# Performance work log

Measured on AMD Instinct MI355X. Metric: run time of the kernel, lower is better.

Reference implementation:

```python
import jax, jax.numpy as jnp
import numpy as np

H, W = 512, 512
G = 8192
ALPHA_THRESH = 1.0 / 255.0        # meta_f32[0]
TRANS_THRESH = 1.0e-4             # meta_f32[1]
ALPHA_CAP = 0.99                  # meta_f32[6]
BG = jnp.zeros((3,), dtype=jnp.float32)  # config.background


def setup_inputs() -> dict:
    key = jax.random.key(0)
    ks = jax.random.split(key, 7)
    mx = jax.random.uniform(ks[0], (G,), minval=0.0, maxval=float(W))
    my = jax.random.uniform(ks[1], (G,), minval=0.0, maxval=float(H))
    means2d = jnp.stack([mx, my], axis=-1)
    # Build valid conics (inverse 2x2 covariances) from random rotation + scales
    theta = jax.random.uniform(ks[2], (G,), minval=0.0, maxval=2.0 * np.pi)
    s = jax.random.uniform(ks[3], (G, 2), minval=2.0, maxval=12.0)  # px stddevs
    ct, st = jnp.cos(theta), jnp.sin(theta)
    v1, v2 = s[:, 0] ** 2, s[:, 1] ** 2
    ca = ct * ct * v1 + st * st * v2
    cb = ct * st * (v1 - v2)
    cc = st * st * v1 + ct * ct * v2
    det = ca * cc - cb * cb
    conics = jnp.stack([cc / det, -cb / det, ca / det], axis=-1)  # [G,3] = (a,b,c)
    colors = jax.random.uniform(ks[4], (G, 3))
    opacities = jax.random.uniform(ks[5], (G,))
    depths = jax.random.uniform(ks[6], (G,), minval=0.1, maxval=100.0)
    return {"means2d": means2d, "conics": conics, "colors": colors,
            "opacities": opacities, "depths": depths}


def reference(means2d, conics, colors, opacities, depths):
    # Stable front-to-back depth sort (mirrors perm = argsort(depths, stable))
    perm = jnp.argsort(depths, stable=True)
    m = means2d[perm]
    cn = conics[perm]
    col = colors[perm]
    op = opacities[perm]
    a, b, c = cn[:, 0], cn[:, 1], cn[:, 2]
    px = jnp.arange(W, dtype=means2d.dtype) + 0.5  # pixel centers

    def row(y):
        py = y.astype(means2d.dtype) + 0.5
        dx = px[:, None] - m[None, :, 0]          # [W,G]
        dy = py - m[:, 1]                          # [G]
        sigma = 0.5 * (a * dx * dx + c * dy * dy) + b * dx * dy  # [W,G]
        alpha = jnp.minimum(ALPHA_CAP, op * jnp.exp(-sigma))
        alpha = jnp.where((sigma < 0) | (alpha < ALPHA_THRESH), 0.0, alpha)
        # exclusive cumulative transmittance along depth order
        Tprev = jnp.cumprod(1.0 - alpha, axis=-1)
        Tprev = jnp.concatenate([jnp.ones((W, 1), alpha.dtype), Tprev[:, :-1]], axis=-1)
        # early-termination: splats seen after T drops below threshold contribute 0
        wgt = alpha * Tprev * (Tprev >= TRANS_THRESH)  # [W,G]
        rgb = wgt @ col                                 # [W,3]
        t_rem = 1.0 - wgt.sum(axis=-1)                  # remaining transmittance
        return rgb + t_rem[:, None] * BG

    return jax.lax.map(row, jnp.arange(H))  # [H,W,3]
```

## Files before the change

kernel.cpp:

```cpp
#include <hip/hip_runtime.h>

#define G 8192
#define IMG_W 512
#define IMG_H 512
#define TILE 16
#define NTX (IMG_W / TILE)
#define NTY (IMG_H / TILE)
#define BLK 256
#define BLKB 64
#define CAP 1024
#define ALPHA_THRESH (1.0f/255.0f)
#define ALPHA_CAP 0.99f
#define TRANS_THRESH 1e-4f

__global__ __launch_bounds__(BLK)
void range_kernel(const float* __restrict__ means2d,
                  const float* __restrict__ conics,
                  const float* __restrict__ colors,
                  const float* __restrict__ opac,
                  unsigned int* __restrict__ ranges,
                  float* __restrict__ tbl)
{
    int g = blockIdx.x * BLK + threadIdx.x;
    if (g >= G) return;
    float op = opac[g];
    float a  = conics[3*g], b = conics[3*g+1], c = conics[3*g+2];
    float mx = means2d[2*g], my = means2d[2*g+1];
    float cr = colors[3*g], cg = colors[3*g+1], cb = colors[3*g+2];

    float4* t4 = (float4*)(tbl + (g << 4));
    t4[0] = make_float4(mx, my, 0.5f * a, b);
    t4[1] = make_float4(0.5f * c, op, cr, cg);
    t4[2] = make_float4(cb, 0.0f, 0.0f, 0.0f);

    unsigned int packed = 0xFFu;
    if (op * 255.0f >= 1.0f) {
        float smax = __logf(op * 255.0f);
        float det = fmaxf(a * c - b * b, 1e-12f);
        float rx = sqrtf(fmaxf(2.0f * smax * c / det, 0.0f)) * 1.0001f + 0.01f;
        float ry = sqrtf(fmaxf(2.0f * smax * a / det, 0.0f)) * 1.0001f + 0.01f;
        int txmin = (int)ceilf ((mx - rx - 15.5f) * 0.0625f);
        int txmax = (int)floorf((mx + rx -  0.5f) * 0.0625f);
        int tymin = (int)ceilf ((my - ry - 15.5f) * 0.0625f);
        int tymax = (int)floorf((my + ry -  0.5f) * 0.0625f);
        if (!(txmax < 0 || txmin > NTX-1 || tymax < 0 || tymin > NTY-1 ||
              txmin > txmax || tymin > tymax)) {
            txmin = max(txmin, 0); txmax = min(txmax, NTX-1);
            tymin = max(tymin, 0); tymax = min(tymax, NTY-1);
            packed = (unsigned)txmin | ((unsigned)txmax << 8)
                   | ((unsigned)tymin << 16) | ((unsigned)tymax << 24);
        }
    }
    ranges[g] = packed;
}

__device__ __forceinline__ int hitp(unsigned p, unsigned btx, unsigned bty)
{
    return (btx >= (p & 0xffu)) & (btx <= ((p >> 8) & 0xffu)) &
           (bty >= ((p >> 16) & 0xffu)) & (bty <= (p >> 24));
}

__global__ __launch_bounds__(BLK)
void tile_kernel(const unsigned int* __restrict__ ranges,
                 const float* __restrict__ depths,
                 const float* __restrict__ tbl,
                 float*       __restrict__ out)
{
    __shared__ __align__(16) unsigned short slist[CAP];
    __shared__ __align__(16) unsigned int fkeys[CAP + 8];
    __shared__ int woff[4];
    __shared__ float4 sq0[4][BLKB];
    __shared__ float4 sq1[4][BLKB];
    __shared__ float  sq2[4][BLKB];
    __shared__ float4 part[4][BLK];

    const int t = threadIdx.x;
    const int lane = t & 63, w = t >> 6;
    const unsigned btx = blockIdx.x, bty = blockIdx.y;

    const uint4* r4 = (const uint4*)ranges;
    const int wbase = w * (G / 4);
    uint4 rv[8];
    #pragma unroll
    for (int i = 0; i < 8; ++i)
        rv[i] = r4[(wbase >> 2) + i * 64 + lane];

    int cnt = 0;
    #pragma unroll
    for (int i = 0; i < 8; ++i)
        cnt += hitp(rv[i].x, btx, bty) + hitp(rv[i].y, btx, bty)
             + hitp(rv[i].z, btx, bty) + hitp(rv[i].w, btx, bty);
    #pragma unroll
    for (int d = 1; d < 64; d <<= 1) cnt += __shfl_xor(cnt, d);
    if (lane == 0) woff[w] = cnt;
    __syncthreads();

    int offs = 0;
    for (int ww = 0; ww < w; ++ww) offs += woff[ww];
    const int N = min(woff[0] + woff[1] + woff[2] + woff[3], CAP);

    const unsigned long long lt = (1ull << lane) - 1ull;
    #pragma unroll
    for (int i = 0; i < 8; ++i) {
        int gbase = wbase + i * 256 + lane * 4;
        int h0 = hitp(rv[i].x, btx, bty), h1 = hitp(rv[i].y, btx, bty);
        int h2 = hitp(rv[i].z, btx, bty), h3 = hitp(rv[i].w, btx, bty);
        unsigned long long m0 = __ballot(h0), m1 = __ballot(h1);
        unsigned long long m2 = __ballot(h2), m3 = __ballot(h3);
        int pos = offs + __popcll(m0 & lt) + __popcll(m1 & lt)
                       + __popcll(m2 & lt) + __popcll(m3 & lt);
        if (h0) { if (pos < CAP) slist[pos] = (unsigned short)(gbase    ); pos++; }
        if (h1) { if (pos < CAP) slist[pos] = (unsigned short)(gbase + 1); pos++; }
        if (h2) { if (pos < CAP) slist[pos] = (unsigned short)(gbase + 2); pos++; }
        if (h3) { if (pos < CAP) slist[pos] = (unsigned short)(gbase + 3); pos++; }
        offs += __popcll(m0) + __popcll(m1) + __popcll(m2) + __popcll(m3);
    }
    __syncthreads();

    unsigned short myidx[4]; unsigned int mykey[4]; int myr[4];
    #pragma unroll
    for (int m = 0; m < 4; ++m) {
        int i = t + m * BLK;
        if (i < N) {
            unsigned idx = slist[i];
            unsigned k = __float_as_uint(depths[idx]);
            myidx[m] = (unsigned short)idx; mykey[m] = k; fkeys[i] = k;
        }
    }
    if (t < 8) fkeys[N + t] = 0xFFFFFFFFu;
    __syncthreads();

    const uint4* fk4 = (const uint4*)fkeys;
    const int nj4 = (N + 3) >> 2;
    #pragma unroll
    for (int m = 0; m < 4; ++m) {
        int i = t + m * BLK;
        if (i < N) {
            unsigned ke = mykey[m]; int r = 0;
            for (int j4 = 0; j4 < nj4; ++j4) {
                uint4 kv = fk4[j4]; int j = j4 << 2;
                r += (int)((kv.x < ke) | ((kv.x == ke) & (j     < i)));
                r += (int)((kv.y < ke) | ((kv.y == ke) & (j + 1 < i)));
                r += (int)((kv.z < ke) | ((kv.z == ke) & (j + 2 < i)));
                r += (int)((kv.w < ke) | ((kv.w == ke) & (j + 3 < i)));
            }
            myr[m] = r;
        }
    }
    __syncthreads();
    #pragma unroll
    for (int m = 0; m < 4; ++m) {
        int i = t + m * BLK;
        if (i < N) slist[myr[m]] = myidx[m];
    }
    __syncthreads();

    const int csz = (N + 3) >> 2;
    const int cs = w * csz;
    const int ce = min(N, cs + csz);

    const float px  = (float)(btx * TILE + (lane & 15)) + 0.5f;
    const int   y0  = (lane >> 4) << 2;
    const float py0 = (float)(bty * TILE + y0) + 0.5f;
    const float py1 = py0 + 1.0f, py2 = py0 + 2.0f, py3 = py0 + 3.0f;

    float T0=1.f,T1=1.f,T2=1.f,T3=1.f;
    float ar0=0.f,ag0=0.f,ab0=0.f, ar1=0.f,ag1=0.f,ab1=0.f;
    float ar2=0.f,ag2=0.f,ab2=0.f, ar3=0.f,ag3=0.f,ab3=0.f;

    for (int base = cs; base < ce; base += BLKB) {
        int k = min(BLKB, ce - base);
        float4 v0 = make_float4(0.f,0.f,0.f,0.f);
        float4 v1 = make_float4(0.f,0.f,0.f,0.f);
        float  v2 = 0.f;
        if (lane < k) {
            int idx = slist[base + lane];
            const float4* b = (const float4*)(tbl + (idx << 4));
            v0 = b[0]; v1 = b[1]; v2 = ((const float*)b)[8];
        }
        sq0[w][lane] = v0; sq1[w][lane] = v1; sq2[w][lane] = v2;
        __threadfence_block();

        int k4 = (k + 3) & ~3;
        bool fin = false;
        for (int i = 0; i < k4; i += 4) {
            #pragma unroll
            for (int u = 0; u < 4; ++u) {
                float4 q0 = sq0[w][i + u];
                float4 q1 = sq1[w][i + u];
                float  bl = sq2[w][i + u];
                float dx = px - q0.x;
                float dxdx = dx * dx;
                float dy0 = py0 - q0.y, dy1 = py1 - q0.y;
                float dy2 = py2 - q0.y, dy3 = py3 - q0.y;
                float sg0 = fmaf(q0.z, dxdx, fmaf(q1.x, dy0*dy0, q0.w*(dx*dy0)));
                float sg1 = fmaf(q0.z, dxdx, fmaf(q1.x, dy1*dy1, q0.w*(dx*dy1)));
                float sg2 = fmaf(q0.z, dxdx, fmaf(q1.x, dy2*dy2, q0.w*(dx*dy2)));
                float sg3 = fmaf(q0.z, dxdx, fmaf(q1.x, dy3*dy3, q0.w*(dx*dy3)));
                float al0 = q1.y * __expf(-sg0);
                float al1 = q1.y * __expf(-sg1);
                float al2 = q1.y * __expf(-sg2);
                float al3 = q1.y * __expf(-sg3);
                al0 = ((sg0 >= 0.f) && (al0 >= ALPHA_THRESH)) ? fminf(al0, ALPHA_CAP) : 0.f;
                al1 = ((sg1 >= 0.f) && (al1 >= ALPHA_THRESH)) ? fminf(al1, ALPHA_CAP) : 0.f;
                al2 = ((sg2 >= 0.f) && (al2 >= ALPHA_THRESH)) ? fminf(al2, ALPHA_CAP) : 0.f;
                al3 = ((sg3 >= 0.f) && (al3 >= ALPHA_THRESH)) ? fminf(al3, ALPHA_CAP) : 0.f;
                float w0 = al0*T0, w1 = al1*T1, w2 = al2*T2, w3 = al3*T3;
                ar0 = fmaf(w0, q1.z, ar0);  ar1 = fmaf(w1, q1.z, ar1);
                ar2 = fmaf(w2, q1.z, ar2);  ar3 = fmaf(w3, q1.z, ar3);
                ag0 = fmaf(w0, q1.w, ag0);  ag1 = fmaf(w1, q1.w, ag1);
                ag2 = fmaf(w2, q1.w, ag2);  ag3 = fmaf(w3, q1.w, ag3);
                ab0 = fmaf(w0, bl,   ab0);  ab1 = fmaf(w1, bl,   ab1);
                ab2 = fmaf(w2, bl,   ab2);  ab3 = fmaf(w3, bl,   ab3);
                T0 *= (1.f - al0);
                T1 *= (1.f - al1);
                T2 *= (1.f - al2);
                T3 *= (1.f - al3);
            }
            if (__all((T0 < TRANS_THRESH) & (T1 < TRANS_THRESH) &
                      (T2 < TRANS_THRESH) & (T3 < TRANS_THRESH))) {
                fin = true; break;
            }
        }
        if (fin) break;
    }

    {
        const int xl = lane & 15;
        part[w][(y0    ) * 16 + xl] = make_float4(ar0, ag0, ab0, T0);
        part[w][(y0 + 1) * 16 + xl] = make_float4(ar1, ag1, ab1, T1);
        part[w][(y0 + 2) * 16 + xl] = make_float4(ar2, ag2, ab2, T2);
        part[w][(y0 + 3) * 16 + xl] = make_float4(ar3, ag3, ab3, T3);
    }
    __syncthreads();

    float4 p0 = part[0][t], p1 = part[1][t], p2 = part[2][t], p3 = part[3][t];
    float r = p3.x, g = p3.y, b = p3.z;
    r = fmaf(p2.w, r, p2.x); g = fmaf(p2.w, g, p2.y); b = fmaf(p2.w, b, p2.z);
    r = fmaf(p1.w, r, p1.x); g = fmaf(p1.w, g, p1.y); b = fmaf(p1.w, b, p1.z);
    r = fmaf(p0.w, r, p0.x); g = fmaf(p0.w, g, p0.y); b = fmaf(p0.w, b, p0.z);

    const int X = (int)btx * TILE + (t & 15);
    const int Y = (int)bty * TILE + (t >> 4);
    const int o = (Y * IMG_W + X) * 3;
    out[o]     = r;
    out[o + 1] = g;
    out[o + 2] = b;
}

extern "C" void kernel_launch(void* const* d_in, const int* in_sizes, int n_in,
                              void* d_out, int out_size, void* d_ws, size_t ws_size,
                              hipStream_t stream)
{
    const float* means2d = (const float*)d_in[0];
    const float* conics  = (const float*)d_in[1];
    const float* colors  = (const float*)d_in[2];
    const float* opac    = (const float*)d_in[3];
    const float* depths  = (const float*)d_in[4];
    float* out = (float*)d_out;
    unsigned int* ranges = (unsigned int*)d_ws;
    float* tbl = (float*)((char*)d_ws + 32 * 1024);

    range_kernel<<<G / BLK, BLK, 0, stream>>>(means2d, conics, colors, opac,
                                              ranges, tbl);
    tile_kernel<<<dim3(NTX, NTY), dim3(BLK), 0, stream>>>(
        ranges, depths, tbl, out);
}
```

Measured before the change: 87.08 us.

## Split tile depth list across eight waves and merge partials in two rounds

```diff
diff --git a/kernel.cpp b/kernel.cpp
--- a/kernel.cpp
+++ b/kernel.cpp
@@ -7,6 +7,7 @@
 #define NTX (IMG_W / TILE)
 #define NTY (IMG_H / TILE)
 #define BLK 256
+#define BLKT 512
 #define BLKB 64
 #define CAP 1024
 #define ALPHA_THRESH (1.0f/255.0f)
@@ -60,34 +61,36 @@
            (bty >= ((p >> 16) & 0xffu)) & (bty <= (p >> 24));
 }
 
-__global__ __launch_bounds__(BLK)
+__global__ __launch_bounds__(BLKT, 8)
 void tile_kernel(const unsigned int* __restrict__ ranges,
                  const float* __restrict__ depths,
                  const float* __restrict__ tbl,
                  float*       __restrict__ out)
 {
     __shared__ __align__(16) unsigned short slist[CAP];
-    __shared__ __align__(16) unsigned int fkeys[CAP + 8];
-    __shared__ int woff[4];
-    __shared__ float4 sq0[4][BLKB];
-    __shared__ float4 sq1[4][BLKB];
-    __shared__ float  sq2[4][BLKB];
-    __shared__ float4 part[4][BLK];
+    __shared__ __align__(16) unsigned char ubuf[BLK * 4 * 16];
+    __shared__ int woff[8];
+    __shared__ __align__(16) float4 sq0[8][BLKB];
+    __shared__ __align__(16) float4 sq1[8][BLKB];
+    __shared__ __align__(16) float  sq2[8][BLKB];
+
+    unsigned int* fkeys = (unsigned int*)ubuf;
+    float4 (*part)[BLK] = (float4 (*)[BLK])ubuf;
 
     const int t = threadIdx.x;
     const int lane = t & 63, w = t >> 6;
     const unsigned btx = blockIdx.x, bty = blockIdx.y;
 
     const uint4* r4 = (const uint4*)ranges;
-    const int wbase = w * (G / 4);
-    uint4 rv[8];
-    #pragma unroll
-    for (int i = 0; i < 8; ++i)
+    const int wbase = w * (G / 8);
+    uint4 rv[4];
+    #pragma unroll
+    for (int i = 0; i < 4; ++i)
         rv[i] = r4[(wbase >> 2) + i * 64 + lane];
 
     int cnt = 0;
     #pragma unroll
-    for (int i = 0; i < 8; ++i)
+    for (int i = 0; i < 4; ++i)
         cnt += hitp(rv[i].x, btx, bty) + hitp(rv[i].y, btx, bty)
              + hitp(rv[i].z, btx, bty) + hitp(rv[i].w, btx, bty);
     #pragma unroll
@@ -97,11 +100,13 @@
 
     int offs = 0;
     for (int ww = 0; ww < w; ++ww) offs += woff[ww];
-    const int N = min(woff[0] + woff[1] + woff[2] + woff[3], CAP);
+    int Nt = 0;
+    for (int ww = 0; ww < 8; ++ww) Nt += woff[ww];
+    const int N = min(Nt, CAP);
 
     const unsigned long long lt = (1ull << lane) - 1ull;
     #pragma unroll
-    for (int i = 0; i < 8; ++i) {
+    for (int i = 0; i < 4; ++i) {
         int gbase = wbase + i * 256 + lane * 4;
         int h0 = hitp(rv[i].x, btx, bty), h1 = hitp(rv[i].y, btx, bty);
         int h2 = hitp(rv[i].z, btx, bty), h3 = hitp(rv[i].w, btx, bty);
@@ -117,10 +122,10 @@
     }
     __syncthreads();
 
-    unsigned short myidx[4]; unsigned int mykey[4]; int myr[4];
-    #pragma unroll
-    for (int m = 0; m < 4; ++m) {
-        int i = t + m * BLK;
+    unsigned short myidx[2]; unsigned int mykey[2]; int myr[2];
+    #pragma unroll
+    for (int m = 0; m < 2; ++m) {
+        int i = t + m * BLKT;
         if (i < N) {
             unsigned idx = slist[i];
             unsigned k = __float_as_uint(depths[idx]);
@@ -133,8 +138,8 @@
     const uint4* fk4 = (const uint4*)fkeys;
     const int nj4 = (N + 3) >> 2;
     #pragma unroll
-    for (int m = 0; m < 4; ++m) {
-        int i = t + m * BLK;
+    for (int m = 0; m < 2; ++m) {
+        int i = t + m * BLKT;
         if (i < N) {
             unsigned ke = mykey[m]; int r = 0;
             for (int j4 = 0; j4 < nj4; ++j4) {
@@ -149,13 +154,13 @@
     }
     __syncthreads();
     #pragma unroll
-    for (int m = 0; m < 4; ++m) {
-        int i = t + m * BLK;
+    for (int m = 0; m < 2; ++m) {
+        int i = t + m * BLKT;
         if (i < N) slist[myr[m]] = myidx[m];
     }
     __syncthreads();
 
-    const int csz = (N + 3) >> 2;
+    const int csz = (N + 7) >> 3;
     const int cs = w * csz;
     const int ce = min(N, cs + csz);
 
@@ -182,7 +187,6 @@
         __threadfence_block();
 
         int k4 = (k + 3) & ~3;
-        bool fin = false;
         for (int i = 0; i < k4; i += 4) {
             #pragma unroll
             for (int u = 0; u < 4; ++u) {
@@ -217,16 +221,13 @@
                 T2 *= (1.f - al2);
                 T3 *= (1.f - al3);
             }
-            if (__all((T0 < TRANS_THRESH) & (T1 < TRANS_THRESH) &
-                      (T2 < TRANS_THRESH) & (T3 < TRANS_THRESH))) {
-                fin = true; break;
-            }
-        }
-        if (fin) break;
-    }
-
-    {
-        const int xl = lane & 15;
+        }
+        if (__all((T0 < TRANS_THRESH) & (T1 < TRANS_THRESH) &
+                  (T2 < TRANS_THRESH) & (T3 < TRANS_THRESH))) break;
+    }
+
+    const int xl = lane & 15;
+    if (w < 4) {
         part[w][(y0    ) * 16 + xl] = make_float4(ar0, ag0, ab0, T0);
         part[w][(y0 + 1) * 16 + xl] = make_float4(ar1, ag1, ab1, T1);
         part[w][(y0 + 2) * 16 + xl] = make_float4(ar2, ag2, ab2, T2);
@@ -234,18 +235,45 @@
     }
     __syncthreads();
 
-    float4 p0 = part[0][t], p1 = part[1][t], p2 = part[2][t], p3 = part[3][t];
-    float r = p3.x, g = p3.y, b = p3.z;
-    r = fmaf(p2.w, r, p2.x); g = fmaf(p2.w, g, p2.y); b = fmaf(p2.w, b, p2.z);
-    r = fmaf(p1.w, r, p1.x); g = fmaf(p1.w, g, p1.y); b = fmaf(p1.w, b, p1.z);
-    r = fmaf(p0.w, r, p0.x); g = fmaf(p0.w, g, p0.y); b = fmaf(p0.w, b, p0.z);
-
-    const int X = (int)btx * TILE + (t & 15);
-    const int Y = (int)bty * TILE + (t >> 4);
-    const int o = (Y * IMG_W + X) * 3;
-    out[o]     = r;
-    out[o + 1] = g;
-    out[o + 2] = b;
+    float cfr=0.f, cfg=0.f, cfb=0.f, tf=1.f;
+    if (t < BLK) {
+        float4 p0 = part[0][t], p1 = part[1][t];
+        float4 p2 = part[2][t], p3 = part[3][t];
+        float r = p3.x, g = p3.y, b = p3.z, T = p3.w;
+        r = fmaf(p2.w, r, p2.x); g = fmaf(p2.w, g, p2.y);
+        b = fmaf(p2.w, b, p2.z); T *= p2.w;
+        r = fmaf(p1.w, r, p1.x); g = fmaf(p1.w, g, p1.y);
+        b = fmaf(p1.w, b, p1.z); T *= p1.w;
+        r = fmaf(p0.w, r, p0.x); g = fmaf(p0.w, g, p0.y);
+        b = fmaf(p0.w, b, p0.z); T *= p0.w;
+        cfr = r; cfg = g; cfb = b; tf = T;
+    }
+    __syncthreads();
+
+    if (w >= 4) {
+        part[w - 4][(y0    ) * 16 + xl] = make_float4(ar0, ag0, ab0, T0);
+        part[w - 4][(y0 + 1) * 16 + xl] = make_float4(ar1, ag1, ab1, T1);
+        part[w - 4][(y0 + 2) * 16 + xl] = make_float4(ar2, ag2, ab2, T2);
+        part[w - 4][(y0 + 3) * 16 + xl] = make_float4(ar3, ag3, ab3, T3);
+    }
+    __syncthreads();
+
+    if (t < BLK) {
+        float4 p0 = part[0][t], p1 = part[1][t];
+        float4 p2 = part[2][t], p3 = part[3][t];
+        float r = p3.x, g = p3.y, b = p3.z;
+        r = fmaf(p2.w, r, p2.x); g = fmaf(p2.w, g, p2.y); b = fmaf(p2.w, b, p2.z);
+        r = fmaf(p1.w, r, p1.x); g = fmaf(p1.w, g, p1.y); b = fmaf(p1.w, b, p1.z);
+        r = fmaf(p0.w, r, p0.x); g = fmaf(p0.w, g, p0.y); b = fmaf(p0.w, b, p0.z);
+        r = fmaf(tf, r, cfr); g = fmaf(tf, g, cfg); b = fmaf(tf, b, cfb);
+
+        const int X = (int)btx * TILE + (t & 15);
+        const int Y = (int)bty * TILE + (t >> 4);
+        const int o = (Y * IMG_W + X) * 3;
+        out[o]     = r;
+        out[o + 1] = g;
+        out[o + 2] = b;
+    }
 }
 
 extern "C" void kernel_launch(void* const* d_in, const int* in_sizes, int n_in,
@@ -263,6 +291,6 @@
 
     range_kernel<<<G / BLK, BLK, 0, stream>>>(means2d, conics, colors, opac,
                                               ranges, tbl);
-    tile_kernel<<<dim3(NTX, NTY), dim3(BLK), 0, stream>>>(
+    tile_kernel<<<dim3(NTX, NTY), dim3(BLKT), 0, stream>>>(
         ranges, depths, tbl, out);
 }
```

Result: slower. 91.19 us (+4.7%).
